# Performance work log

Measured on AMD Instinct MI355X. Metric: run time of the kernel, lower is better.

## Reference

```python
import jax, jax.numpy as jnp
import numpy as np

D = 512          # input_dim == hidden size of MinLSTM layers
OUT = 1          # output_dim of fc_out
B, T = 8, 4096
LN_EPS = 1e-5


def _linear_params(key, d_in, d_out):
    kw, kb = jax.random.split(key)
    lim = 1.0 / np.sqrt(d_in)
    W = jax.random.uniform(kw, (d_out, d_in), minval=-lim, maxval=lim, dtype=jnp.float32)
    b = jax.random.uniform(kb, (d_out,), minval=-lim, maxval=lim, dtype=jnp.float32)
    return W, b


def setup_inputs() -> dict:
    key = jax.random.key(0)
    ks = jax.random.split(key, 8)
    x = jax.random.normal(ks[0], (B, T, D), dtype=jnp.float32)
    Wf0, bf0 = _linear_params(ks[1], D, D)
    Wi0, bi0 = _linear_params(ks[2], D, D)
    Wh0, bh0 = _linear_params(ks[3], D, D)
    Wf1, bf1 = _linear_params(ks[4], D, D)
    Wi1, bi1 = _linear_params(ks[5], D, D)
    Wh1, bh1 = _linear_params(ks[6], D, D)
    W_out, b_out = _linear_params(ks[7], D, OUT)
    ln_g = jnp.ones((D,), dtype=jnp.float32)
    ln_b = jnp.zeros((D,), dtype=jnp.float32)
    return {
        'x': x,
        'Wf0': Wf0, 'bf0': bf0, 'Wi0': Wi0, 'bi0': bi0, 'Wh0': Wh0, 'bh0': bh0,
        'Wf1': Wf1, 'bf1': bf1, 'Wi1': Wi1, 'bi1': bi1, 'Wh1': Wh1, 'bh1': bh1,
        'ln_g': ln_g, 'ln_b': ln_b, 'W_out': W_out, 'b_out': b_out,
    }


def _minlstm(x, Wf, bf, Wi, bi, Wh, bh):
    # minLSTM (parallel form, h0 = 0):
    #   f = sigma(W_f x), i = sigma(W_i x), h~ = W_h x
    #   f' = f/(f+i), i' = i/(f+i)
    #   h_t = f'_t * h_{t-1} + i'_t * h~_t   (linear recurrence -> associative scan)
    f = jax.nn.sigmoid(jnp.einsum('btd,ed->bte', x, Wf) + bf)
    i = jax.nn.sigmoid(jnp.einsum('btd,ed->bte', x, Wi) + bi)
    h_tilde = jnp.einsum('btd,ed->bte', x, Wh) + bh
    denom = f + i
    a = f / denom                      # decay coefficient f'
    u = (i / denom) * h_tilde          # input contribution i' * h~

    def combine(c1, c2):
        a1, u1 = c1
        a2, u2 = c2
        return a1 * a2, a2 * u1 + u2

    _, h = jax.lax.associative_scan(combine, (a, u), axis=1)
    return h  # [B, T, D]


def reference(x, Wf0, bf0, Wi0, bi0, Wh0, bh0,
              Wf1, bf1, Wi1, bi1, Wh1, bh1,
              ln_g, ln_b, W_out, b_out):
    h = _minlstm(x, Wf0, bf0, Wi0, bi0, Wh0, bh0)
    h = _minlstm(h, Wf1, bf1, Wi1, bi1, Wh1, bh1)
    h = jnp.where(jnp.isnan(h), x, h)      # NaN fallback to input
    h = x + h                               # residual
    # LayerNorm over last dim
    mu = jnp.mean(h, axis=-1, keepdims=True)
    var = jnp.mean(jnp.square(h - mu), axis=-1, keepdims=True)
    hn = (h - mu) * jax.lax.rsqrt(var + LN_EPS) * ln_g + ln_b
    # output projection [B, T, OUT]
    return jnp.einsum('btd,od->bto', hn, W_out) + b_out
```

## Files before the change

### kernel.cpp

```cpp
#include <hip/hip_runtime.h>
#include <hip/hip_bf16.h>
#include <stdint.h>


#define MROWS 32768
#define DDIM  512
#define TLEN  4096
#define BSZ   8
#define NCHUNK 64
#define CLEN   64

typedef __attribute__((ext_vector_type(8))) __bf16 bf16x8;
typedef __attribute__((ext_vector_type(16))) float f32x16;
typedef __attribute__((ext_vector_type(4))) unsigned short ushort4_t;

static __device__ __forceinline__ unsigned short f2bf(float f) {
    unsigned int u = __float_as_uint(f);
    u = (u + 0x7FFFu + ((u >> 16) & 1u)) >> 16;
    return (unsigned short)u;
}
static __device__ __forceinline__ float bf2f(unsigned short s) {
    return __uint_as_float(((unsigned int)s) << 16);
}
static __device__ __forceinline__ void gload_lds16(const void* gptr, void* ldsp) {
    __builtin_amdgcn_global_load_lds(
        (const __attribute__((address_space(1))) uint32_t*)gptr,
        (__attribute__((address_space(3))) uint32_t*)ldsp,
        16, 0, 0);
}

#define WAITV(n) asm volatile("s_waitcnt vmcnt(" #n ")" ::: "memory")

__global__ __launch_bounds__(256) void cast_all(
    const float4* __restrict__ x,
    const float4* __restrict__ w0, const float4* __restrict__ w1,
    const float4* __restrict__ w2, const float4* __restrict__ w3,
    const float4* __restrict__ w4, const float4* __restrict__ w5,
    ushort4_t* __restrict__ xb, ushort4_t* __restrict__ wb)
{
    int i = blockIdx.x * 256 + threadIdx.x;
    float4 v;
    ushort4_t* dst;
    if (i < 4194304) {
        v = x[i];
        dst = xb + i;
    } else {
        int j = i - 4194304;
        int wsel = j >> 16;
        int rem = j & 65535;
        const float4* src = (wsel == 0) ? w0 : (wsel == 1) ? w1 : (wsel == 2) ? w2
                          : (wsel == 3) ? w3 : (wsel == 4) ? w4 : w5;
        v = src[rem];
        dst = wb + j;
    }
    ushort4_t o;
    o.x = f2bf(v.x); o.y = f2bf(v.y); o.z = f2bf(v.z); o.w = f2bf(v.w);
    *dst = o;
}

__global__ __launch_bounds__(256, 2) void gates_gemm(
    const unsigned short* __restrict__ X,
    const unsigned short* __restrict__ Wf,
    const unsigned short* __restrict__ Wi,
    const unsigned short* __restrict__ Wh,
    const float* __restrict__ bf_, const float* __restrict__ bi_,
    const float* __restrict__ bh_,
    unsigned int* __restrict__ au_out,
    float* __restrict__ Asum, float* __restrict__ Usum)
{
    __shared__ __align__(16) unsigned short lds[3 * 10240];

    const int tid  = threadIdx.x;
    const int lane = tid & 63;
    const int wave = tid >> 6;
    const int wm = wave >> 1;
    const int wn = wave & 1;
    const int ln31 = lane & 31;
    const int kh = lane >> 5;

    const int w = blockIdx.x;
    const int xcd = w & 7;
    const int s = w >> 3;
    const int by = xcd * 32 + (s >> 3);
    const int bx = s & 7;
    const int mblk = by * 128;
    const int nblk = bx * 64;

    const int srow = tid >> 2;
    const int c4   = tid & 3;
    const int cg   = ((c4 ^ (((srow >> 1) ^ (srow >> 3)) & 3)) << 3);
    const int tid8 = tid * 8;
    const unsigned short* g0 = X  + (size_t)(mblk + srow) * 512 + cg;
    const unsigned short* g1 = X  + (size_t)(mblk + 64 + srow) * 512 + cg;
    const unsigned short* g2 = Wf + (size_t)(nblk + srow) * 512 + cg;
    const unsigned short* g3 = Wi + (size_t)(nblk + srow) * 512 + cg;
    const unsigned short* g4 = Wh + (size_t)(nblk + srow) * 512 + cg;

    const int fl = ((ln31 >> 1) ^ (ln31 >> 3)) & 3;
    int aoff[2][2], boff[2];
#pragma unroll
    for (int mi = 0; mi < 2; ++mi) {
        int row = wm * 64 + mi * 32 + ln31;
#pragma unroll
        for (int ks = 0; ks < 2; ++ks)
            aoff[mi][ks] = row * 32 + (((2 * ks + kh) ^ fl) << 3);
    }
    {
        int brow = wn * 32 + ln31;
#pragma unroll
        for (int ks = 0; ks < 2; ++ks)
            boff[ks] = brow * 32 + (((2 * ks + kh) ^ fl) << 3);
    }

    f32x16 accF[2], accI[2], accH[2];
#pragma unroll
    for (int mi = 0; mi < 2; ++mi) {
#pragma unroll
        for (int e = 0; e < 16; ++e) { accF[mi][e] = 0.f; accI[mi][e] = 0.f; accH[mi][e] = 0.f; }
    }

#define STAGE(bb) do { \
    gload_lds16(g0, lds + (bb) + tid8);            \
    gload_lds16(g1, lds + (bb) + 2048 + tid8);     \
    gload_lds16(g2, lds + (bb) + 4096 + tid8);     \
    gload_lds16(g3, lds + (bb) + 6144 + tid8);     \
    gload_lds16(g4, lds + (bb) + 8192 + tid8);     \
    g0 += 32; g1 += 32; g2 += 32; g3 += 32; g4 += 32; } while (0)

    STAGE(0);
    STAGE(10240);

#pragma unroll
    for (int t = 0; t < 16; ++t) {
        if (t < 15) { WAITV(5); }
        else        { WAITV(0); }
        __builtin_amdgcn_s_barrier();
        __builtin_amdgcn_sched_barrier(0);

        if (t < 14) STAGE(((t + 2) % 3) * 10240);

        const unsigned short* cb = lds + (t % 3) * 10240;
#pragma unroll
        for (int ks = 0; ks < 2; ++ks) {
            bf16x8 af0 = *reinterpret_cast<const bf16x8*>(cb + aoff[0][ks]);
            bf16x8 bF  = *reinterpret_cast<const bf16x8*>(cb + 4096 + boff[ks]);
            bf16x8 af1 = *reinterpret_cast<const bf16x8*>(cb + aoff[1][ks]);
            bf16x8 bI  = *reinterpret_cast<const bf16x8*>(cb + 6144 + boff[ks]);
            bf16x8 bH  = *reinterpret_cast<const bf16x8*>(cb + 8192 + boff[ks]);
            __builtin_amdgcn_s_setprio(1);
            accF[0] = __builtin_amdgcn_mfma_f32_32x32x16_bf16(af0, bF, accF[0], 0, 0, 0);
            accF[1] = __builtin_amdgcn_mfma_f32_32x32x16_bf16(af1, bF, accF[1], 0, 0, 0);
            accI[0] = __builtin_amdgcn_mfma_f32_32x32x16_bf16(af0, bI, accI[0], 0, 0, 0);
            accI[1] = __builtin_amdgcn_mfma_f32_32x32x16_bf16(af1, bI, accI[1], 0, 0, 0);
            accH[0] = __builtin_amdgcn_mfma_f32_32x32x16_bf16(af0, bH, accH[0], 0, 0, 0);
            accH[1] = __builtin_amdgcn_mfma_f32_32x32x16_bf16(af1, bH, accH[1], 0, 0, 0);
            __builtin_amdgcn_s_setprio(0);
        }
        __builtin_amdgcn_sched_barrier(0);
    }
#undef STAGE

    const int n = nblk + wn * 32 + ln31;
    const float bfv = bf_[n], biv = bi_[n], bhv = bh_[n];
    const bool up = (lane & 32) != 0;
    float ca = 1.f, cu = 0.f;
#pragma unroll
    for (int mi = 0; mi < 2; ++mi) {
#pragma unroll
        for (int j = 0; j < 4; ++j) {
            float sa = 1.f, su = 0.f;
#pragma unroll
            for (int r = 0; r < 4; ++r) {
                const int reg = 4 * j + r;
                const int m = mblk + wm * 64 + mi * 32 + 8 * j + 4 * kh + r;
                float zf = accF[mi][reg] + bfv;
                float zi = accI[mi][reg] + biv;
                float zh = accH[mi][reg] + bhv;
                float ef = __expf(-zf);
                float ei = __expf(-zi);
                float inv = __frcp_rn(2.0f + ef + ei);
                float av = (1.0f + ei) * inv;
                float uv = (1.0f + ef) * inv * zh;
                au_out[(size_t)m * 512 + n] =
                    ((unsigned int)f2bf(uv) << 16) | (unsigned int)f2bf(av);
                su = av * su + uv; sa *= av;
            }
            float oa = __shfl_xor(sa, 32), ou = __shfl_xor(su, 32);
            float ta = sa * oa;
            float tu = up ? (sa * ou + su) : (oa * su + ou);
            cu = ta * cu + tu; ca = ca * ta;
        }
    }
    if (lane < 32) {
        size_t ci = (size_t)(by * 2 + wm) * 512 + n;
        Asum[ci] = ca;
        Usum[ci] = cu;
    }
}

__global__ void scan_pass2(const float4* __restrict__ Asum, const float4* __restrict__ Usum,
                           float4* __restrict__ Hinit) {
    int t = blockIdx.x * 256 + threadIdx.x;
    int d4 = t & 127;
    int b = t >> 7;
    float4 h = {0.f, 0.f, 0.f, 0.f};
    for (int c = 0; c < NCHUNK; ++c) {
        size_t idx = (size_t)(b * NCHUNK + c) * 128 + d4;
        Hinit[idx] = h;
        float4 A = Asum[idx]; float4 U = Usum[idx];
        h.x = A.x * h.x + U.x; h.y = A.y * h.y + U.y;
        h.z = A.z * h.z + U.z; h.w = A.w * h.w + U.w;
    }
}

__global__ void scan_pass3(const uint4* __restrict__ au,
                           const float4* __restrict__ Hinit,
                           ushort4_t* __restrict__ hout) {
    int gid = blockIdx.x * 256 + threadIdx.x;
    int d4 = gid & 127;
    int c  = (gid >> 7) & 63;
    int b  = gid >> 13;
    size_t base = (size_t)(b * TLEN + c * CLEN) * 128 + d4;
    size_t s4 = (size_t)(b * NCHUNK + c) * 128 + d4;
    float4 h0 = Hinit[s4];
    float h[4] = {h0.x, h0.y, h0.z, h0.w};
#pragma unroll 4
    for (int l = 0; l < CLEN; ++l) {
        size_t idx = base + (size_t)l * 128;
        uint4 v = au[idx];
        unsigned int vv[4] = {v.x, v.y, v.z, v.w};
        ushort4_t o;
#pragma unroll
        for (int j = 0; j < 4; ++j) {
            float av = __uint_as_float(vv[j] << 16);
            float uv = __uint_as_float(vv[j] & 0xFFFF0000u);
            h[j] = av * h[j] + uv;
            o[j] = f2bf(h[j]);
        }
        hout[idx] = o;
    }
}

__global__ __launch_bounds__(128) void scan3_final(
    const uint4* __restrict__ au, const float4* __restrict__ Hinit,
    const float4* __restrict__ x4,
    const float* __restrict__ g, const float* __restrict__ bvec,
    const float* __restrict__ Wout, const float* __restrict__ bout,
    float* __restrict__ out)
{
    const int blk = blockIdx.x;
    const int b = blk >> 6, c = blk & 63;
    const int d4 = threadIdx.x;
    const int lane = threadIdx.x & 63;
    const int wv = threadIdx.x >> 6;

    float4 h0 = Hinit[(size_t)blk * 128 + d4];
    float h[4] = {h0.x, h0.y, h0.z, h0.w};
    float4 g4 = reinterpret_cast<const float4*>(g)[d4];
    float4 b4 = reinterpret_cast<const float4*>(bvec)[d4];
    float4 w4 = reinterpret_cast<const float4*>(Wout)[d4];
    const float ga[4] = {g4.x, g4.y, g4.z, g4.w};
    const float ba[4] = {b4.x, b4.y, b4.z, b4.w};
    const float wa[4] = {w4.x, w4.y, w4.z, w4.w};
    const float bo = bout[0];

    __shared__ float redS[2], redQ[2], redP[2];
    size_t base = ((size_t)b * TLEN + c * CLEN) * 128 + d4;

    for (int l = 0; l < CLEN; ++l) {
        size_t idx = base + (size_t)l * 128;
        uint4 v = au[idx];
        float4 xr = x4[idx];
        const unsigned int vv[4] = {v.x, v.y, v.z, v.w};
        const float xa[4] = {xr.x, xr.y, xr.z, xr.w};
        float r[4];
        float sfl = 0.f, q = 0.f;
#pragma unroll
        for (int j = 0; j < 4; ++j) {
            float av = __uint_as_float(vv[j] << 16);
            float uv = __uint_as_float(vv[j] & 0xFFFF0000u);
            h[j] = av * h[j] + uv;
            float hv = h[j];
            if (hv != hv) hv = xa[j];
            float rr = xa[j] + hv;
            r[j] = rr;
            sfl += rr; q += rr * rr;
        }
#pragma unroll
        for (int m = 32; m >= 1; m >>= 1) {
            sfl += __shfl_xor(sfl, m);
            q += __shfl_xor(q, m);
        }
        if (lane == 0) { redS[wv] = sfl; redQ[wv] = q; }
        __syncthreads();
        float st = redS[0] + redS[1];
        float qt = redQ[0] + redQ[1];
        float mu = st * (1.0f / 512.0f);
        float var = qt * (1.0f / 512.0f) - mu * mu;
        float rstd = rsqrtf(var + 1e-5f);
        float p = 0.f;
#pragma unroll
        for (int j = 0; j < 4; ++j)
            p += ((r[j] - mu) * rstd * ga[j] + ba[j]) * wa[j];
#pragma unroll
        for (int m = 32; m >= 1; m >>= 1) p += __shfl_xor(p, m);
        if (lane == 0) redP[wv] = p;
        __syncthreads();
        if (threadIdx.x == 0)
            out[(size_t)b * TLEN + c * CLEN + l] = redP[0] + redP[1] + bo;
    }
}

extern "C" void kernel_launch(void* const* d_in, const int* in_sizes, int n_in,
                              void* d_out, int out_size, void* d_ws, size_t ws_size,
                              hipStream_t stream) {
    const float* x    = (const float*)d_in[0];
    const float* Wf0  = (const float*)d_in[1];  const float* bf0 = (const float*)d_in[2];
    const float* Wi0  = (const float*)d_in[3];  const float* bi0 = (const float*)d_in[4];
    const float* Wh0  = (const float*)d_in[5];  const float* bh0 = (const float*)d_in[6];
    const float* Wf1  = (const float*)d_in[7];  const float* bf1 = (const float*)d_in[8];
    const float* Wi1  = (const float*)d_in[9];  const float* bi1 = (const float*)d_in[10];
    const float* Wh1  = (const float*)d_in[11]; const float* bh1 = (const float*)d_in[12];
    const float* ln_g = (const float*)d_in[13]; const float* ln_b = (const float*)d_in[14];
    const float* W_out = (const float*)d_in[15]; const float* b_out = (const float*)d_in[16];

    char* ws = (char*)d_ws;
    unsigned short* Xb = (unsigned short*)ws;  ws += (size_t)MROWS * DDIM * 2;
    unsigned short* Wball = (unsigned short*)ws;
    unsigned short* Wb[6];
    for (int i = 0; i < 6; ++i) { Wb[i] = (unsigned short*)ws; ws += (size_t)DDIM * DDIM * 2; }
    unsigned int* aubuf = (unsigned int*)ws; ws += (size_t)MROWS * DDIM * 4;
    float* Asum = (float*)ws;  ws += (size_t)BSZ * NCHUNK * DDIM * 4;
    float* Usum = (float*)ws;  ws += (size_t)BSZ * NCHUNK * DDIM * 4;
    float* Hinit = (float*)ws; ws += (size_t)BSZ * NCHUNK * DDIM * 4;
    unsigned short* h0b = (unsigned short*)ws; ws += (size_t)MROWS * DDIM * 2;

    cast_all<<<17920, 256, 0, stream>>>(
        (const float4*)x, (const float4*)Wf0, (const float4*)Wi0, (const float4*)Wh0,
        (const float4*)Wf1, (const float4*)Wi1, (const float4*)Wh1,
        (ushort4_t*)Xb, (ushort4_t*)Wball);

    gates_gemm<<<2048, 256, 0, stream>>>(Xb, Wb[0], Wb[1], Wb[2], bf0, bi0, bh0,
                                         aubuf, Asum, Usum);
    scan_pass2<<<4, 256, 0, stream>>>((const float4*)Asum, (const float4*)Usum, (float4*)Hinit);
    scan_pass3<<<256, 256, 0, stream>>>((const uint4*)aubuf, (const float4*)Hinit, (ushort4_t*)h0b);

    gates_gemm<<<2048, 256, 0, stream>>>(h0b, Wb[3], Wb[4], Wb[5], bf1, bi1, bh1,
                                         aubuf, Asum, Usum);
    scan_pass2<<<4, 256, 0, stream>>>((const float4*)Asum, (const float4*)Usum, (float4*)Hinit);
    scan3_final<<<512, 128, 0, stream>>>((const uint4*)aubuf, (const float4*)Hinit,
                                         (const float4*)x, ln_g, ln_b, W_out, b_out,
                                         (float*)d_out);
}
```

Before: 246.6 us.

## Switch gates GEMM to K=64 tiles with double buffering

The gates GEMM main loop changes from 16 iterations of K=32 with a triple-buffered LDS ring to 8 iterations of K=64 with two buffers of twice the size. The XOR swizzle is reworked for 64-element rows, and each thread now issues 10 global-to-LDS loads per stage. Each iteration now prefetches the next stage before waiting and adds a trailing barrier so a buffer is not overwritten while other waves still read it. This cuts the number of barrier and wait rounds, but the prefetch distance drops to one stage and there are two barriers per iteration. LDS use rises from 60 KB to 80 KB, which may limit the declared occupancy of 2 blocks per CU.

Result: no change. 243.2 us (-1.4%).

```diff
diff --git a/kernel.cpp b/kernel.cpp
--- a/kernel.cpp
+++ b/kernel.cpp
@@ -68,7 +68,7 @@
     unsigned int* __restrict__ au_out,
     float* __restrict__ Asum, float* __restrict__ Usum)
 {
-    __shared__ __align__(16) unsigned short lds[3 * 10240];
+    __shared__ __align__(16) unsigned short lds[2 * 20480];
 
     const int tid  = threadIdx.x;
     const int lane = tid & 63;
@@ -86,67 +86,72 @@
     const int mblk = by * 128;
     const int nblk = bx * 64;
 
-    const int srow = tid >> 2;
-    const int c4   = tid & 3;
-    const int cg   = ((c4 ^ (((srow >> 1) ^ (srow >> 3)) & 3)) << 3);
+    const int srow = tid >> 3;
+    const int c8   = tid & 7;
+    const int cg   = (c8 ^ (srow & 7)) << 3;
     const int tid8 = tid * 8;
-    const unsigned short* g0 = X  + (size_t)(mblk + srow) * 512 + cg;
-    const unsigned short* g1 = X  + (size_t)(mblk + 64 + srow) * 512 + cg;
-    const unsigned short* g2 = Wf + (size_t)(nblk + srow) * 512 + cg;
-    const unsigned short* g3 = Wi + (size_t)(nblk + srow) * 512 + cg;
-    const unsigned short* g4 = Wh + (size_t)(nblk + srow) * 512 + cg;
-
-    const int fl = ((ln31 >> 1) ^ (ln31 >> 3)) & 3;
-    int aoff[2][2], boff[2];
+    const unsigned short* gA0 = X + (size_t)(mblk + srow) * 512 + cg;
+    const unsigned short* gA1 = X + (size_t)(mblk + 32 + srow) * 512 + cg;
+    const unsigned short* gA2 = X + (size_t)(mblk + 64 + srow) * 512 + cg;
+    const unsigned short* gA3 = X + (size_t)(mblk + 96 + srow) * 512 + cg;
+    const unsigned short* gF0 = Wf + (size_t)(nblk + srow) * 512 + cg;
+    const unsigned short* gF1 = Wf + (size_t)(nblk + 32 + srow) * 512 + cg;
+    const unsigned short* gI0 = Wi + (size_t)(nblk + srow) * 512 + cg;
+    const unsigned short* gI1 = Wi + (size_t)(nblk + 32 + srow) * 512 + cg;
+    const unsigned short* gH0 = Wh + (size_t)(nblk + srow) * 512 + cg;
+    const unsigned short* gH1 = Wh + (size_t)(nblk + 32 + srow) * 512 + cg;
+
+    const int fl = ln31 & 7;
+    int co[4];
+#pragma unroll
+    for (int ks = 0; ks < 4; ++ks)
+        co[ks] = ((2 * ks + kh) ^ fl) << 3;
+    const int abase0 = (wm * 64 + ln31) * 64;
+    const int abase1 = (wm * 64 + 32 + ln31) * 64;
+    const int bbase  = 8192 + (wn * 32 + ln31) * 64;
+
+    f32x16 accF[2], accI[2], accH[2];
 #pragma unroll
     for (int mi = 0; mi < 2; ++mi) {
-        int row = wm * 64 + mi * 32 + ln31;
-#pragma unroll
-        for (int ks = 0; ks < 2; ++ks)
-            aoff[mi][ks] = row * 32 + (((2 * ks + kh) ^ fl) << 3);
-    }
-    {
-        int brow = wn * 32 + ln31;
-#pragma unroll
-        for (int ks = 0; ks < 2; ++ks)
-            boff[ks] = brow * 32 + (((2 * ks + kh) ^ fl) << 3);
-    }
-
-    f32x16 accF[2], accI[2], accH[2];
-#pragma unroll
-    for (int mi = 0; mi < 2; ++mi) {
 #pragma unroll
         for (int e = 0; e < 16; ++e) { accF[mi][e] = 0.f; accI[mi][e] = 0.f; accH[mi][e] = 0.f; }
     }
 
 #define STAGE(bb) do { \
-    gload_lds16(g0, lds + (bb) + tid8);            \
-    gload_lds16(g1, lds + (bb) + 2048 + tid8);     \
-    gload_lds16(g2, lds + (bb) + 4096 + tid8);     \
-    gload_lds16(g3, lds + (bb) + 6144 + tid8);     \
-    gload_lds16(g4, lds + (bb) + 8192 + tid8);     \
-    g0 += 32; g1 += 32; g2 += 32; g3 += 32; g4 += 32; } while (0)
+    gload_lds16(gA0, lds + (bb) + tid8);             \
+    gload_lds16(gA1, lds + (bb) + 2048  + tid8);     \
+    gload_lds16(gA2, lds + (bb) + 4096  + tid8);     \
+    gload_lds16(gA3, lds + (bb) + 6144  + tid8);     \
+    gload_lds16(gF0, lds + (bb) + 8192  + tid8);     \
+    gload_lds16(gF1, lds + (bb) + 10240 + tid8);     \
+    gload_lds16(gI0, lds + (bb) + 12288 + tid8);     \
+    gload_lds16(gI1, lds + (bb) + 14336 + tid8);     \
+    gload_lds16(gH0, lds + (bb) + 16384 + tid8);     \
+    gload_lds16(gH1, lds + (bb) + 18432 + tid8);     \
+    gA0 += 64; gA1 += 64; gA2 += 64; gA3 += 64; gF0 += 64; \
+    gF1 += 64; gI0 += 64; gI1 += 64; gH0 += 64; gH1 += 64; } while (0)
 
     STAGE(0);
-    STAGE(10240);
-
-#pragma unroll
-    for (int t = 0; t < 16; ++t) {
-        if (t < 15) { WAITV(5); }
-        else        { WAITV(0); }
+
+#pragma unroll
+    for (int t = 0; t < 8; ++t) {
+        if (t < 7) {
+            STAGE(((t + 1) & 1) * 20480);
+            WAITV(10);
+        } else {
+            WAITV(0);
+        }
         __builtin_amdgcn_s_barrier();
         __builtin_amdgcn_sched_barrier(0);
 
-        if (t < 14) STAGE(((t + 2) % 3) * 10240);
-
-        const unsigned short* cb = lds + (t % 3) * 10240;
-#pragma unroll
-        for (int ks = 0; ks < 2; ++ks) {
-            bf16x8 af0 = *reinterpret_cast<const bf16x8*>(cb + aoff[0][ks]);
-            bf16x8 bF  = *reinterpret_cast<const bf16x8*>(cb + 4096 + boff[ks]);
-            bf16x8 af1 = *reinterpret_cast<const bf16x8*>(cb + aoff[1][ks]);
-            bf16x8 bI  = *reinterpret_cast<const bf16x8*>(cb + 6144 + boff[ks]);
-            bf16x8 bH  = *reinterpret_cast<const bf16x8*>(cb + 8192 + boff[ks]);
+        const unsigned short* cb = lds + (t & 1) * 20480;
+#pragma unroll
+        for (int ks = 0; ks < 4; ++ks) {
+            bf16x8 af0 = *reinterpret_cast<const bf16x8*>(cb + abase0 + co[ks]);
+            bf16x8 bF  = *reinterpret_cast<const bf16x8*>(cb + bbase + co[ks]);
+            bf16x8 af1 = *reinterpret_cast<const bf16x8*>(cb + abase1 + co[ks]);
+            bf16x8 bI  = *reinterpret_cast<const bf16x8*>(cb + bbase + 4096 + co[ks]);
+            bf16x8 bH  = *reinterpret_cast<const bf16x8*>(cb + bbase + 8192 + co[ks]);
             __builtin_amdgcn_s_setprio(1);
             accF[0] = __builtin_amdgcn_mfma_f32_32x32x16_bf16(af0, bF, accF[0], 0, 0, 0);
             accF[1] = __builtin_amdgcn_mfma_f32_32x32x16_bf16(af1, bF, accF[1], 0, 0, 0);
@@ -156,6 +161,8 @@
             accH[1] = __builtin_amdgcn_mfma_f32_32x32x16_bf16(af1, bH, accH[1], 0, 0, 0);
             __builtin_amdgcn_s_setprio(0);
         }
+        __builtin_amdgcn_sched_barrier(0);
+        __builtin_amdgcn_s_barrier();
         __builtin_amdgcn_sched_barrier(0);
     }
 #undef STAGE
```
